# Kernel tuning notes

Measured on AMD Instinct MI355X. Metric: run time of the kernel, lower is better.

The kernel has to match this reference:

```python
import jax, jax.numpy as jnp
import numpy as np

N_NODES = 2097152  # total nodes
HIDDEN = 64        # feature dim D

def setup_inputs() -> dict:
    key = jax.random.key(0)
    features = jax.random.normal(key, (N_NODES, HIDDEN), dtype=jnp.float32)
    return {"features": features, "n_per_graph": 512}

def reference(features, n_per_graph):
    # features: [N, D]; N = B * n_per_graph (uniform segments)
    N, D = features.shape
    B = N // n_per_graph
    X = features.reshape(B, n_per_graph, D)          # [B, n, D]
    mu = jnp.mean(X, axis=1, keepdims=True)          # [B, 1, D]
    Xc = X - mu                                      # mean-centered
    # per-graph covariance: (Xc^T Xc) / n  -> [B, D, D]
    cov = jnp.einsum('bnd,bne->bde', Xc, Xc) / jnp.asarray(n_per_graph, X.dtype)
    iu0, iu1 = jnp.triu_indices(D)                   # upper triangle incl. diag
    return cov[:, iu0, iu1]                          # [B, D*(D+1)/2]
```

## Files before the change

kernel.cpp:

```cpp
#include <hip/hip_runtime.h>
#include <hip/hip_bf16.h>


#define DD      64
#define NPG     512
#define CHUNK   256
#define XSTRIDE 264

typedef __bf16 bf16x8 __attribute__((ext_vector_type(8)));
typedef float  f32x4  __attribute__((ext_vector_type(4)));

__device__ __forceinline__ unsigned int f2bf_pack(float a, float b) {
  unsigned int ua = __builtin_bit_cast(unsigned int, a);
  unsigned int ub = __builtin_bit_cast(unsigned int, b);
  ua = ua + 0x7fffu + ((ua >> 16) & 1u);
  ub = ub + 0x7fffu + ((ub >> 16) & 1u);
  return (ua >> 16) | (ub & 0xffff0000u);
}

__global__ __launch_bounds__(256, 4)
void cov_pool_kernel(const float* __restrict__ X, float* __restrict__ out) {
  __shared__ __align__(16) unsigned short Xt[DD * XSTRIDE];
  __shared__ float sumbuf[4][DD];
  __shared__ float mu[DD];

  const int t    = threadIdx.x;
  const int lane = t & 63;
  const int w    = t >> 6;
  const long g   = blockIdx.x;
  const float* Xg = X + g * (long)(NPG * DD);

  const int dimq = lane & 15;
  const int kgrp = (lane >> 4) * 8;

  float csum = 0.f;
  f32x4 acc[4];
  f32x4 zero = {0.f, 0.f, 0.f, 0.f};
  acc[0] = zero; acc[1] = zero; acc[2] = zero; acc[3] = zero;

  for (int half = 0; half < 2; ++half) {
    #pragma unroll 4
    for (int it = 0; it < CHUNK / 16; ++it) {
      const int nc = it * 16 + w * 4;
      const int n  = half * CHUNK + nc;
      const float* p = Xg + (long)n * DD + lane;
      float f0 = p[0];
      float f1 = p[DD];
      float f2 = p[2 * DD];
      float f3 = p[3 * DD];
      csum += (f0 + f1) + (f2 + f3);
      uint2 v;
      v.x = f2bf_pack(f0, f1);
      v.y = f2bf_pack(f2, f3);
      *(uint2*)&Xt[lane * XSTRIDE + nc] = v;
    }
    __syncthreads();

    #pragma unroll 2
    for (int kk = 0; kk < CHUNK / 32; ++kk) {
      const int kb = kk * 32 + kgrp;
      const bf16x8 A   = *(const bf16x8*)&Xt[(w * 16 + dimq) * XSTRIDE + kb];
      const bf16x8 fb0 = *(const bf16x8*)&Xt[( 0 + dimq) * XSTRIDE + kb];
      const bf16x8 fb1 = *(const bf16x8*)&Xt[(16 + dimq) * XSTRIDE + kb];
      const bf16x8 fb2 = *(const bf16x8*)&Xt[(32 + dimq) * XSTRIDE + kb];
      const bf16x8 fb3 = *(const bf16x8*)&Xt[(48 + dimq) * XSTRIDE + kb];
      if (w <= 0) acc[0] = __builtin_amdgcn_mfma_f32_16x16x32_bf16(A, fb0, acc[0], 0, 0, 0);
      if (w <= 1) acc[1] = __builtin_amdgcn_mfma_f32_16x16x32_bf16(A, fb1, acc[1], 0, 0, 0);
      if (w <= 2) acc[2] = __builtin_amdgcn_mfma_f32_16x16x32_bf16(A, fb2, acc[2], 0, 0, 0);
      acc[3] = __builtin_amdgcn_mfma_f32_16x16x32_bf16(A, fb3, acc[3], 0, 0, 0);
    }
    __syncthreads();
  }

  sumbuf[w][lane] = csum;
  __syncthreads();
  if (t < DD) {
    mu[t] = (sumbuf[0][t] + sumbuf[1][t] + sumbuf[2][t] + sumbuf[3][t]) * (1.f / NPG);
  }
  __syncthreads();

  const float inv_n = 1.f / NPG;
  float* og = out + g * 2080L;
  const int rbase = w * 16 + (lane >> 4) * 4;
  #pragma unroll
  for (int tn = 0; tn < 4; ++tn) {
    if (tn < w) continue;
    const int j = tn * 16 + dimq;
    const float muj = mu[j];
    #pragma unroll
    for (int r = 0; r < 4; ++r) {
      const int i = rbase + r;
      if (j >= i) {
        const float v = acc[tn][r] * inv_n - mu[i] * muj;
        og[i * DD - (i * (i - 1)) / 2 + (j - i)] = v;
      }
    }
  }
}

extern "C" void kernel_launch(void* const* d_in, const int* in_sizes, int n_in,
                              void* d_out, int out_size, void* d_ws, size_t ws_size,
                              hipStream_t stream) {
  const float* X = (const float*)d_in[0];
  float* out = (float*)d_out;
  const int N = in_sizes[0] / DD;
  const int B = N / NPG;
  cov_pool_kernel<<<dim3(B), dim3(256), 0, stream>>>(X, out);
}
```

Measured before the change: 116.0 us.

## Halve LDS chunk to raise occupancy and widen bf16 staging stores

Shrinks the shared-memory staging chunk from 256 to 128 nodes, iterated four times, and raises the launch-bounds occupancy hint from 4 to 8 blocks per CU. Each thread now loads 8 rows and writes one 16-byte bf16x8 vector to LDS instead of two 4-byte packs. Float-to-bf16 conversion moves from a manual bit-rounding helper to native casts. This aims at more blocks in flight to hide global-load latency, at the cost of twice as many barriers per graph and possible register pressure under the tighter bound.

```diff
diff --git a/kernel.cpp b/kernel.cpp
--- a/kernel.cpp
+++ b/kernel.cpp
@@ -4,21 +4,13 @@
 
 #define DD      64
 #define NPG     512
-#define CHUNK   256
-#define XSTRIDE 264
+#define CHUNK   128
+#define XSTRIDE 136
 
 typedef __bf16 bf16x8 __attribute__((ext_vector_type(8)));
 typedef float  f32x4  __attribute__((ext_vector_type(4)));
 
-__device__ __forceinline__ unsigned int f2bf_pack(float a, float b) {
-  unsigned int ua = __builtin_bit_cast(unsigned int, a);
-  unsigned int ub = __builtin_bit_cast(unsigned int, b);
-  ua = ua + 0x7fffu + ((ua >> 16) & 1u);
-  ub = ub + 0x7fffu + ((ub >> 16) & 1u);
-  return (ua >> 16) | (ub & 0xffff0000u);
-}
-
-__global__ __launch_bounds__(256, 4)
+__global__ __launch_bounds__(256, 8)
 void cov_pool_kernel(const float* __restrict__ X, float* __restrict__ out) {
   __shared__ __align__(16) unsigned short Xt[DD * XSTRIDE];
   __shared__ float sumbuf[4][DD];
@@ -28,7 +20,7 @@
   const int lane = t & 63;
   const int w    = t >> 6;
   const long g   = blockIdx.x;
-  const float* Xg = X + g * (long)(NPG * DD);
+  const float* Xg = X + g * (long)(NPG * DD) + lane;
 
   const int dimq = lane & 15;
   const int kgrp = (lane >> 4) * 8;
@@ -38,25 +30,23 @@
   f32x4 zero = {0.f, 0.f, 0.f, 0.f};
   acc[0] = zero; acc[1] = zero; acc[2] = zero; acc[3] = zero;
 
-  for (int half = 0; half < 2; ++half) {
-    #pragma unroll 4
-    for (int it = 0; it < CHUNK / 16; ++it) {
-      const int nc = it * 16 + w * 4;
-      const int n  = half * CHUNK + nc;
-      const float* p = Xg + (long)n * DD + lane;
-      float f0 = p[0];
-      float f1 = p[DD];
-      float f2 = p[2 * DD];
-      float f3 = p[3 * DD];
-      csum += (f0 + f1) + (f2 + f3);
-      uint2 v;
-      v.x = f2bf_pack(f0, f1);
-      v.y = f2bf_pack(f2, f3);
-      *(uint2*)&Xt[lane * XSTRIDE + nc] = v;
+  for (int c = 0; c < NPG / CHUNK; ++c) {
+    #pragma unroll
+    for (int it = 0; it < CHUNK / 32; ++it) {
+      const int nc = it * 32 + w * 8;
+      const float* p = Xg + (long)(c * CHUNK + nc) * DD;
+      float f[8];
+      #pragma unroll
+      for (int k = 0; k < 8; ++k) f[k] = p[k * DD];
+      csum += ((f[0] + f[1]) + (f[2] + f[3])) + ((f[4] + f[5]) + (f[6] + f[7]));
+      bf16x8 b;
+      #pragma unroll
+      for (int k = 0; k < 8; ++k) b[k] = (__bf16)f[k];
+      *(bf16x8*)&Xt[lane * XSTRIDE + nc] = b;
     }
     __syncthreads();
 
-    #pragma unroll 2
+    #pragma unroll
     for (int kk = 0; kk < CHUNK / 32; ++kk) {
       const int kb = kk * 32 + kgrp;
       const bf16x8 A   = *(const bf16x8*)&Xt[(w * 16 + dimq) * XSTRIDE + kb];
```

New measurement: 322.2 us. 2.78x slower.
